# Optimization experiments

Measured on AMD Instinct MI355X. Metric: run time of the kernel, lower is better.

## Reference

```python
import jax, jax.numpy as jnp
import numpy as np

G = 200          # voxel grid extent per axis (spatial_shape)
EPS = 1e-5       # BatchNorm eps


def setup_inputs() -> dict:
    N, C_in, C_out = 1_000_000, 6, 32
    rng = np.random.default_rng(0)
    # unique active voxel sites (submanifold conv assumes deduplicated coords)
    lin = rng.choice(G ** 3, size=N, replace=False)
    coords = np.stack([lin // (G * G), (lin // G) % G, lin % G], axis=1).astype(np.int32)
    key = jax.random.key(0)
    k1, k2 = jax.random.split(key)
    feat = jax.random.normal(k1, (N, C_in), jnp.float32)
    W = jax.random.normal(k2, (27, C_in, C_out), jnp.float32) * (1.0 / np.sqrt(27 * C_in))
    gamma = jnp.ones((C_out,), jnp.float32)
    beta = jnp.zeros((C_out,), jnp.float32)
    return {"feat": feat, "coords": jnp.asarray(coords), "W": W, "gamma": gamma, "beta": beta}


def _subm_conv_bn_relu(feat, coords, W, gamma, beta):
    # Submanifold 3x3x3 sparse conv: output only at active sites.
    N = feat.shape[0]
    c = coords
    keys = (c[:, 0] * G + c[:, 1]) * G + c[:, 2]          # linearized voxel keys
    order = jnp.argsort(keys)
    skeys = keys[order]
    sfeat = feat[order]
    # all 27 kernel offsets, center included
    r = jnp.arange(-1, 2, dtype=c.dtype)
    offs = jnp.stack(jnp.meshgrid(r, r, r, indexing="ij"), -1).reshape(27, 3)

    def step(acc, xs):
        off, Wk = xs                                       # off: [3], Wk: [C_in, C_out]
        nc = c + off                                       # neighbor coords [N,3]
        valid = jnp.all((nc >= 0) & (nc < G), axis=1)
        nkey = (nc[:, 0] * G + nc[:, 1]) * G + nc[:, 2]
        pos = jnp.clip(jnp.searchsorted(skeys, nkey), 0, N - 1)
        found = valid & (skeys[pos] == nkey)               # rulebook hit mask
        g = jnp.where(found[:, None], sfeat[pos], 0.0)     # gathered neighbor feats [N,C_in]
        return acc + g @ Wk, None

    out, _ = jax.lax.scan(step, jnp.zeros((N, W.shape[2]), feat.dtype), (offs, W))
    # BatchNorm1d (training-mode batch stats) + ReLU
    mean = out.mean(0)
    var = out.var(0)
    out = (out - mean) * jax.lax.rsqrt(var + EPS) * gamma + beta
    return jax.nn.relu(out)


def reference(feat, coords, W, gamma, beta):
    return _subm_conv_bn_relu(feat, coords, W, gamma, beta)
```

## Files before the change

### kernel.cpp

```cpp
#include <hip/hip_runtime.h>
#include <stdint.h>

#define GRIDX 200
#define P 202
#define PCELL (P * P * P)
#define GUARD 100000
#define NBITS (PCELL + GUARD)
#define NWP ((NBITS + 31) / 32)
#define K_INV (PCELL + 50000)
#define CIN 6
#define COUT 32
#define NOFF 27
#define BN_EPS 1e-5f
#define WPB 1024
#define NBLKP ((NWP + WPB - 1) / WPB)

typedef __attribute__((ext_vector_type(8))) short short8;
typedef __attribute__((ext_vector_type(4))) float f32x4;


__device__ __forceinline__ int xcd_swizzle(int b, int nwg) {
    int q = nwg >> 3, r = nwg & 7;
    int xcd = b & 7, idx = b >> 3;
    int base = (xcd < r) ? xcd * (q + 1) : r * (q + 1) + (xcd - r) * q;
    return base + idx;
}

__device__ __forceinline__ unsigned short f2bf(float f) {
    uint32_t u = __float_as_uint(f);
    return (unsigned short)((u + 0x7FFFu + ((u >> 16) & 1u)) >> 16);
}
__device__ __forceinline__ uint32_t pack2(float a, float b) {
    return (uint32_t)f2bf(a) | ((uint32_t)f2bf(b) << 16);
}

__device__ __forceinline__ int koff_delta(int koff) {
    int t9 = koff / 9;
    int r9 = koff - t9 * 9;
    int t3 = r9 / 3;
    return (t9 - 1) * (P * P) + (t3 - 1) * P + (r9 - t3 * 3 - 1);
}


__global__ void build_bitmap_p(const int* __restrict__ coords, int N,
                               uint2* __restrict__ recs) {
    int i = blockIdx.x * blockDim.x + threadIdx.x;
    if (i >= N) return;
    int x = coords[3 * i], y = coords[3 * i + 1], z = coords[3 * i + 2];
    int key = ((x + 1) * P + (y + 1)) * P + (z + 1);
    atomicOr((unsigned int*)&recs[key >> 5], 1u << (key & 31));
}

__global__ __launch_bounds__(256)
void bitmap_count_p(const uint2* __restrict__ recs, int* __restrict__ bcnt) {
    __shared__ int tot[256];
    int b = blockIdx.x, t = threadIdx.x;
    int w0 = b * WPB + t * 4;
    int s = 0;
#pragma unroll
    for (int j = 0; j < 4; j++) {
        int w = w0 + j;
        if (w < NWP) s += __popc(recs[w].x);
    }
    tot[t] = s;
    __syncthreads();
    if (t < 128) tot[t] += tot[t + 128];
    __syncthreads();
    if (t < 64) {
        int v = tot[t] + tot[t + 64];
#pragma unroll
        for (int d = 32; d > 0; d >>= 1) v += __shfl_down(v, d);
        if (t == 0) bcnt[b] = v;
    }
}

__global__ void scan_small(const int* __restrict__ cnt, int* __restrict__ base, int n) {
    __shared__ int tot[256];
    int t = threadIdx.x;
    int v = (t < n) ? cnt[t] : 0;
    tot[t] = v;
    __syncthreads();
    for (int d = 1; d < 256; d <<= 1) {
        int u = (t >= d) ? tot[t - d] : 0;
        __syncthreads();
        tot[t] += u;
        __syncthreads();
    }
    if (t < n) base[t] = tot[t] - v;
}

__global__ __launch_bounds__(256)
void base_fill_p(uint2* __restrict__ recs, const int* __restrict__ bbase) {
    __shared__ int tot[256];
    int b = blockIdx.x, t = threadIdx.x;
    int w0 = b * WPB + t * 4;
    int p[4];
    int s = 0;
#pragma unroll
    for (int j = 0; j < 4; j++) {
        int w = w0 + j;
        p[j] = (w < NWP) ? __popc(recs[w].x) : 0;
        s += p[j];
    }
    tot[t] = s;
    __syncthreads();
    for (int d = 1; d < 256; d <<= 1) {
        int u = (t >= d) ? tot[t - d] : 0;
        __syncthreads();
        tot[t] += u;
        __syncthreads();
    }
    int run = bbase[b] + tot[t] - s;
#pragma unroll
    for (int j = 0; j < 4; j++) {
        int w = w0 + j;
        if (w < NWP) recs[w].y = (uint32_t)run;
        run += p[j];
    }
}


__global__ __launch_bounds__(256)
void gen_skeys(const uint2* __restrict__ recs, int* __restrict__ skeys) {
    int w = blockIdx.x * blockDim.x + threadIdx.x;
    if (w >= NWP) return;
    uint2 rb = recs[w];
    uint32_t m = rb.x;
    int base = (int)rb.y;
    int key0 = w * 32;
    while (m) {
        int bit = __ffs((int)m) - 1;
        skeys[base++] = key0 + bit;
        m &= m - 1u;
    }
}


__global__ __launch_bounds__(256)
void rank_scatter_p(const int* __restrict__ coords, const float* __restrict__ feat, int N,
                    const uint2* __restrict__ recs,
                    int* __restrict__ sorig,
                    uint4* __restrict__ feat_bf) {
    int i = blockIdx.x * blockDim.x + threadIdx.x;
    if (i >= N) return;
    int x = coords[3 * i], y = coords[3 * i + 1], z = coords[3 * i + 2];
    int key = ((x + 1) * P + (y + 1)) * P + (z + 1);
    uint2 rb = recs[key >> 5];
    int bit = key & 31;
    int r = (int)(rb.y + (uint32_t)__popc(rb.x & ((1u << bit) - 1u)));
    sorig[r] = i;
    const float* fr = feat + (size_t)i * CIN;
    float2 a = *(const float2*)fr;
    float2 bb = *(const float2*)(fr + 2);
    float2 cc = *(const float2*)(fr + 4);
    uint4 u;
    u.x = pack2(a.x, a.y);
    u.y = pack2(bb.x, bb.y);
    u.z = pack2(cc.x, cc.y);
    u.w = 0u;
    feat_bf[r] = u;
}


__global__ void prep_wfrag(const float* __restrict__ W, uint4* __restrict__ wfrag) {
    int idx = blockIdx.x * blockDim.x + threadIdx.x;
    if (idx >= 7 * 2 * 64) return;
    int l = idx & 63;
    int nt = (idx >> 6) & 1;
    int ks = idx >> 7;
    int koff = (l >> 4) * 7 + ks;
    int col = nt * 16 + (l & 15);
    unsigned short v[8];
#pragma unroll
    for (int ci = 0; ci < 8; ci++) {
        float f = 0.f;
        if (ci < CIN && koff < NOFF) f = W[(koff * CIN + ci) * COUT + col];
        v[ci] = f2bf(f);
    }
    uint4 u;
    u.x = (uint32_t)v[0] | ((uint32_t)v[1] << 16);
    u.y = (uint32_t)v[2] | ((uint32_t)v[3] << 16);
    u.z = (uint32_t)v[4] | ((uint32_t)v[5] << 16);
    u.w = (uint32_t)v[6] | ((uint32_t)v[7] << 16);
    wfrag[idx] = u;
}


__global__ __launch_bounds__(256, 4)
void conv_mfma(const uint4* __restrict__ feat_bf,
               const int* __restrict__ skeys,
               const int* __restrict__ sorig,
               const uint4* __restrict__ wfrag,
               const uint2* __restrict__ recs, int N, int nsb,
               float* __restrict__ out,
               float* __restrict__ stats_g) {
    __shared__ __align__(16) float Clds[64 * 36];
    __shared__ float bstat[64];

    int tid = threadIdx.x;
    int w = tid >> 6, l = tid & 63;
    int col = l & 15;
    int rg = l >> 4;
    int kb = rg;

    if (tid < 64) bstat[tid] = 0.f;

    const short8* wf8 = (const short8*)wfrag;
    short8 bf0[7], bf1[7];
#pragma unroll
    for (int ks = 0; ks < 7; ks++) {
        bf0[ks] = wf8[(ks * 2 + 0) * 64 + l];
        bf1[ks] = wf8[(ks * 2 + 1) * 64 + l];
    }

    int b1 = (0x3123 >> (kb * 4)) & 0xF;
    int b2 = b1 + 3;
    int len0 = b1, len2 = 4 - b1;
    int koffC0 = kb * 7;
    int koffC1 = koffC0 + b1;
    int koffC2 = koffC0 + b2;
    int d0 = koff_delta(koffC0);
    int d1 = koff_delta(koffC1);
    bool padC2 = (koffC2 >= NOFF);
    int d2 = padC2 ? 0 : koff_delta(koffC2);

    const uint4* fb16 = (const uint4*)feat_bf;

    float as0 = 0.f, aq0 = 0.f, as1 = 0.f, aq1 = 0.f;

    for (int sb = blockIdx.x; sb < nsb; sb += gridDim.x) {
        int b = xcd_swizzle(sb, nsb);
        int bs = b * 64;
        int site = bs + w * 16 + col;
        int key = (site < N) ? skeys[site] : K_INV;

        int nkA = key + d0;
        int nkB = key + d1;
        int nkC = padC2 ? K_INV : key + d2;
        int waA = nkA >> 5, waB = nkB >> 5, waC = nkC >> 5;
        uint2 rA0 = recs[waA];
        uint2 rB0 = recs[waB];
        uint2 rC0 = recs[waC];
        uint2 rA1 = rA0, rB1 = rB0, rC1 = rC0;
        if (((nkA & 31) + len0) > 32) rA1 = recs[waA + 1];
        if (((nkB & 31) + 3) > 32)    rB1 = recs[waB + 1];
        if (((nkC & 31) + len2) > 32) rC1 = recs[waC + 1];

        short8 av[7];
#pragma unroll
        for (int ks = 0; ks < 7; ks++) {
            int c = (ks >= b1) + (ks >= b2);
            int nk = (c == 0) ? (nkA + ks)
                   : (c == 1) ? (nkB + (ks - b1))
                              : (nkC + (ks - b2));
            int wa  = (c == 0) ? waA : (c == 1) ? waB : waC;
            uint2 r0 = (c == 0) ? rA0 : (c == 1) ? rB0 : rC0;
            uint2 r1 = (c == 0) ? rA1 : (c == 1) ? rB1 : rC1;
            bool second = (nk >> 5) != wa;
            uint32_t wd = second ? r1.x : r0.x;
            uint32_t bw = second ? r1.y : r0.y;
            int p = nk & 31;
            bool hit = (wd >> p) & 1u;
            uint4 a4 = make_uint4(0u, 0u, 0u, 0u);
            if (hit) {
                int pos = (int)(bw + (uint32_t)__popc(wd & ((1u << p) - 1u)));
                a4 = fb16[pos];
            }
            av[ks] = *(const short8*)&a4;
        }

        f32x4 acc0 = {0.f, 0.f, 0.f, 0.f};
        f32x4 acc1 = {0.f, 0.f, 0.f, 0.f};
#pragma unroll
        for (int ks = 0; ks < 7; ks++) {
            acc0 = __builtin_amdgcn_mfma_f32_16x16x32_bf16(av[ks], bf0[ks], acc0, 0, 0, 0);
            acc1 = __builtin_amdgcn_mfma_f32_16x16x32_bf16(av[ks], bf1[ks], acc1, 0, 0, 0);
        }

        as0 += acc0[0] + acc0[1] + acc0[2] + acc0[3];
        aq0 += acc0[0]*acc0[0] + acc0[1]*acc0[1] + acc0[2]*acc0[2] + acc0[3]*acc0[3];
        as1 += acc1[0] + acc1[1] + acc1[2] + acc1[3];
        aq1 += acc1[0]*acc1[0] + acc1[1]*acc1[1] + acc1[2]*acc1[2] + acc1[3]*acc1[3];

        __syncthreads();
#pragma unroll
        for (int r = 0; r < 4; r++) {
            int s = w * 16 + rg * 4 + r;
            Clds[s * 36 + col] = acc0[r];
            Clds[s * 36 + col + 16] = acc1[r];
        }
        __syncthreads();

        int st = tid >> 2;
        int q = (tid & 3) * 2;
        int sr = bs + st;
        if (sr < N) {
            float4* gp = (float4*)(out + (size_t)sorig[sr] * COUT + q * 4);
            gp[0] = *(const float4*)&Clds[st * 36 + q * 4];
            gp[1] = *(const float4*)&Clds[st * 36 + q * 4 + 4];
        }
    }

    as0 += __shfl_xor(as0, 16); as0 += __shfl_xor(as0, 32);
    aq0 += __shfl_xor(aq0, 16); aq0 += __shfl_xor(aq0, 32);
    as1 += __shfl_xor(as1, 16); as1 += __shfl_xor(as1, 32);
    aq1 += __shfl_xor(aq1, 16); aq1 += __shfl_xor(aq1, 32);
    __syncthreads();
    if (l < 16) {
        atomicAdd(&bstat[col], as0);
        atomicAdd(&bstat[16 + col], as1);
        atomicAdd(&bstat[32 + col], aq0);
        atomicAdd(&bstat[48 + col], aq1);
    }
    __syncthreads();
    if (tid < 64) {
        int slice = blockIdx.x & 63;
        atomicAdd(&stats_g[slice * 64 + tid], bstat[tid]);
    }
}


__global__ void finalize_sliced(const float* __restrict__ stats_g,
                                const float* __restrict__ gamma,
                                const float* __restrict__ beta,
                                float invN, float* __restrict__ scsh) {
    int c = threadIdx.x;
    if (c < COUT) {
        float s = 0.f, q = 0.f;
        for (int sl = 0; sl < 64; sl++) {
            s += stats_g[sl * 64 + c];
            q += stats_g[sl * 64 + 32 + c];
        }
        float mean = s * invN;
        float var = q * invN - mean * mean;
        float sc = gamma[c] * rsqrtf(var + BN_EPS);
        scsh[c] = sc;
        scsh[COUT + c] = beta[c] - mean * sc;
    }
}

__global__ __launch_bounds__(256)
void norm_kernel(float* __restrict__ out, long total_vec,
                 const float* __restrict__ scaleshift) {
    __shared__ float sc[COUT], sh[COUT];
    for (int t = threadIdx.x; t < COUT; t += blockDim.x) {
        sc[t] = scaleshift[t];
        sh[t] = scaleshift[COUT + t];
    }
    __syncthreads();
    long stride = (long)gridDim.x * blockDim.x;
    float4* p = (float4*)out;
    for (long v = (long)blockIdx.x * blockDim.x + threadIdx.x; v < total_vec; v += stride) {
        int cbase = (int)(v & 7) * 4;
        float4 u = p[v];
        u.x = fmaxf(u.x * sc[cbase + 0] + sh[cbase + 0], 0.f);
        u.y = fmaxf(u.y * sc[cbase + 1] + sh[cbase + 1], 0.f);
        u.z = fmaxf(u.z * sc[cbase + 2] + sh[cbase + 2], 0.f);
        u.w = fmaxf(u.w * sc[cbase + 3] + sh[cbase + 3], 0.f);
        p[v] = u;
    }
}


extern "C" void kernel_launch(void* const* d_in, const int* in_sizes, int n_in,
                              void* d_out, int out_size, void* d_ws, size_t ws_size,
                              hipStream_t stream) {
    const float* feat   = (const float*)d_in[0];
    const int*   coords = (const int*)d_in[1];
    const float* W      = (const float*)d_in[2];
    const float* gamma  = (const float*)d_in[3];
    const float* beta   = (const float*)d_in[4];
    float* out = (float*)d_out;

    int N = in_sizes[0] / CIN;
    const int threads = 256;
    int blocksN = (N + threads - 1) / threads;
    int nsb = (N + 63) / 64;
    int cblocks = 1024;
    long total_vec = (long)N * COUT / 4;

    size_t a256 = 255;
    size_t recs_b     = (size_t)NWP * 8;
    size_t off_skeys  = (recs_b + a256) & ~a256;
    size_t off_featbf = (off_skeys + (size_t)N * 4 + a256) & ~a256;
    size_t off_sorig  = (off_featbf + (size_t)(N + 1) * 16 + a256) & ~a256;
    size_t off_bcnt   = (off_sorig + (size_t)N * 4 + a256) & ~a256;
    size_t off_bbase  = (off_bcnt + 256 * 4 + a256) & ~a256;
    size_t off_wfrag  = (off_bbase + 256 * 4 + a256) & ~a256;
    size_t off_stats  = (off_wfrag + (size_t)(7 * 2 * 64) * 16 + a256) & ~a256;
    size_t off_scsh   = off_stats + (size_t)64 * 64 * 4;

    uint2* recs  = (uint2*)d_ws;
    int*   skeys = (int*)((char*)d_ws + off_skeys);
    uint4* featb = (uint4*)((char*)d_ws + off_featbf);
    int*   sorig = (int*)((char*)d_ws + off_sorig);
    int*   bcnt  = (int*)((char*)d_ws + off_bcnt);
    int*   bbase = (int*)((char*)d_ws + off_bbase);
    uint4* wfrag = (uint4*)((char*)d_ws + off_wfrag);
    float* stats = (float*)((char*)d_ws + off_stats);
    float* scsh  = (float*)((char*)d_ws + off_scsh);

    hipMemsetAsync(recs, 0, recs_b, stream);
    hipMemsetAsync(stats, 0, (size_t)64 * 64 * 4, stream);
    prep_wfrag<<<4, threads, 0, stream>>>(W, wfrag);
    build_bitmap_p<<<blocksN, threads, 0, stream>>>(coords, N, recs);
    bitmap_count_p<<<NBLKP, threads, 0, stream>>>(recs, bcnt);
    scan_small<<<1, threads, 0, stream>>>(bcnt, bbase, NBLKP);
    base_fill_p<<<NBLKP, threads, 0, stream>>>(recs, bbase);
    gen_skeys<<<(NWP + threads - 1) / threads, threads, 0, stream>>>(recs, skeys);
    rank_scatter_p<<<blocksN, threads, 0, stream>>>(coords, feat, N, recs, sorig, featb);
    conv_mfma<<<cblocks, threads, 0, stream>>>(featb, skeys, sorig, wfrag, recs, N, nsb, out, stats);
    finalize_sliced<<<1, 64, 0, stream>>>(stats, gamma, beta, 1.0f / (float)N, scsh);
    norm_kernel<<<2048, threads, 0, stream>>>(out, total_vec, scsh);
}
```

Baseline: 195.9 us.

## Fuse skey generation into base fill, vectorize coord/feat loads, merge memsets

Moves sorted-key emission into the prefix-sum base_fill kernel, which removes the separate gen_skeys launch and its reread of the bitmap. The bitmap build and rank-scatter kernels now have each thread handle 4 points using int4/float4 vector loads. The workspace is reordered so the bitmap and BN stats are contiguous, which lets a single memset zero both. The cost is more per-thread serial work in base_fill (each thread walks up to 4 words) and fewer threads in the scatter kernels.

```diff
diff --git a/kernel.cpp b/kernel.cpp
--- a/kernel.cpp
+++ b/kernel.cpp
@@ -42,13 +42,29 @@
 }
 
 
-__global__ void build_bitmap_p(const int* __restrict__ coords, int N,
-                               uint2* __restrict__ recs) {
-    int i = blockIdx.x * blockDim.x + threadIdx.x;
-    if (i >= N) return;
-    int x = coords[3 * i], y = coords[3 * i + 1], z = coords[3 * i + 2];
-    int key = ((x + 1) * P + (y + 1)) * P + (z + 1);
-    atomicOr((unsigned int*)&recs[key >> 5], 1u << (key & 31));
+__global__ __launch_bounds__(256)
+void build_bitmap_v4(const int* __restrict__ coords, int N, uint2* __restrict__ recs) {
+    int t = blockIdx.x * blockDim.x + threadIdx.x;
+    int i0 = t * 4;
+    if (i0 >= N) return;
+    if (i0 + 4 <= N) {
+        const int4* c4 = (const int4*)(coords + (size_t)i0 * 3);
+        int4 ca = c4[0], cb = c4[1], cc = c4[2];
+        int cx[4] = {ca.x, ca.w, cb.z, cc.y};
+        int cy[4] = {ca.y, cb.x, cb.w, cc.z};
+        int cz[4] = {ca.z, cb.y, cc.x, cc.w};
+#pragma unroll
+        for (int s = 0; s < 4; s++) {
+            int key = ((cx[s] + 1) * P + (cy[s] + 1)) * P + (cz[s] + 1);
+            atomicOr((unsigned int*)&recs[key >> 5], 1u << (key & 31));
+        }
+    } else {
+        for (int i = i0; i < N; i++) {
+            int x = coords[3 * i], y = coords[3 * i + 1], z = coords[3 * i + 2];
+            int key = ((x + 1) * P + (y + 1)) * P + (z + 1);
+            atomicOr((unsigned int*)&recs[key >> 5], 1u << (key & 31));
+        }
+    }
 }
 
 __global__ __launch_bounds__(256)
@@ -90,16 +106,19 @@
 }
 
 __global__ __launch_bounds__(256)
-void base_fill_p(uint2* __restrict__ recs, const int* __restrict__ bbase) {
+void base_fill_skeys(uint2* __restrict__ recs, const int* __restrict__ bbase,
+                     int* __restrict__ skeys) {
     __shared__ int tot[256];
     int b = blockIdx.x, t = threadIdx.x;
     int w0 = b * WPB + t * 4;
+    uint32_t wd[4];
     int p[4];
     int s = 0;
 #pragma unroll
     for (int j = 0; j < 4; j++) {
         int w = w0 + j;
-        p[j] = (w < NWP) ? __popc(recs[w].x) : 0;
+        wd[j] = (w < NWP) ? recs[w].x : 0u;
+        p[j] = __popc(wd[j]);
         s += p[j];
     }
     tot[t] = s;
@@ -114,51 +133,73 @@
 #pragma unroll
     for (int j = 0; j < 4; j++) {
         int w = w0 + j;
-        if (w < NWP) recs[w].y = (uint32_t)run;
-        run += p[j];
+        if (w < NWP) {
+            recs[w].y = (uint32_t)run;
+            uint32_t m = wd[j];
+            int rr = run;
+            int k0 = w * 32;
+            while (m) {
+                int bit = __ffs((int)m) - 1;
+                skeys[rr++] = k0 + bit;
+                m &= m - 1u;
+            }
+            run += p[j];
+        }
     }
 }
 
 
 __global__ __launch_bounds__(256)
-void gen_skeys(const uint2* __restrict__ recs, int* __restrict__ skeys) {
-    int w = blockIdx.x * blockDim.x + threadIdx.x;
-    if (w >= NWP) return;
-    uint2 rb = recs[w];
-    uint32_t m = rb.x;
-    int base = (int)rb.y;
-    int key0 = w * 32;
-    while (m) {
-        int bit = __ffs((int)m) - 1;
-        skeys[base++] = key0 + bit;
-        m &= m - 1u;
-    }
-}
-
-
-__global__ __launch_bounds__(256)
-void rank_scatter_p(const int* __restrict__ coords, const float* __restrict__ feat, int N,
-                    const uint2* __restrict__ recs,
-                    int* __restrict__ sorig,
-                    uint4* __restrict__ feat_bf) {
-    int i = blockIdx.x * blockDim.x + threadIdx.x;
-    if (i >= N) return;
-    int x = coords[3 * i], y = coords[3 * i + 1], z = coords[3 * i + 2];
-    int key = ((x + 1) * P + (y + 1)) * P + (z + 1);
-    uint2 rb = recs[key >> 5];
-    int bit = key & 31;
-    int r = (int)(rb.y + (uint32_t)__popc(rb.x & ((1u << bit) - 1u)));
-    sorig[r] = i;
-    const float* fr = feat + (size_t)i * CIN;
-    float2 a = *(const float2*)fr;
-    float2 bb = *(const float2*)(fr + 2);
-    float2 cc = *(const float2*)(fr + 4);
-    uint4 u;
-    u.x = pack2(a.x, a.y);
-    u.y = pack2(bb.x, bb.y);
-    u.z = pack2(cc.x, cc.y);
-    u.w = 0u;
-    feat_bf[r] = u;
+void rank_scatter_v4(const int* __restrict__ coords, const float* __restrict__ feat, int N,
+                     const uint2* __restrict__ recs,
+                     int* __restrict__ sorig, uint4* __restrict__ feat_bf) {
+    int t = blockIdx.x * blockDim.x + threadIdx.x;
+    int i0 = t * 4;
+    if (i0 >= N) return;
+    if (i0 + 4 <= N) {
+        const int4* c4 = (const int4*)(coords + (size_t)i0 * 3);
+        int4 ca = c4[0], cb = c4[1], cc = c4[2];
+        int cx[4] = {ca.x, ca.w, cb.z, cc.y};
+        int cy[4] = {ca.y, cb.x, cb.w, cc.z};
+        int cz[4] = {ca.z, cb.y, cc.x, cc.w};
+        const float4* f4 = (const float4*)(feat + (size_t)i0 * 6);
+        float4 fa = f4[0], fb = f4[1], fc = f4[2], fd = f4[3], fe = f4[4], ff = f4[5];
+        float fs[4][6] = {
+            {fa.x, fa.y, fa.z, fa.w, fb.x, fb.y},
+            {fb.z, fb.w, fc.x, fc.y, fc.z, fc.w},
+            {fd.x, fd.y, fd.z, fd.w, fe.x, fe.y},
+            {fe.z, fe.w, ff.x, ff.y, ff.z, ff.w}};
+#pragma unroll
+        for (int s = 0; s < 4; s++) {
+            int key = ((cx[s] + 1) * P + (cy[s] + 1)) * P + (cz[s] + 1);
+            uint2 rb = recs[key >> 5];
+            int bit = key & 31;
+            int r = (int)(rb.y + (uint32_t)__popc(rb.x & ((1u << bit) - 1u)));
+            sorig[r] = i0 + s;
+            uint4 u;
+            u.x = pack2(fs[s][0], fs[s][1]);
+            u.y = pack2(fs[s][2], fs[s][3]);
+            u.z = pack2(fs[s][4], fs[s][5]);
+            u.w = 0u;
+            feat_bf[r] = u;
+        }
+    } else {
+        for (int i = i0; i < N; i++) {
+            int x = coords[3 * i], y = coords[3 * i + 1], z = coords[3 * i + 2];
+            int key = ((x + 1) * P + (y + 1)) * P + (z + 1);
+            uint2 rb = recs[key >> 5];
+            int bit = key & 31;
+            int r = (int)(rb.y + (uint32_t)__popc(rb.x & ((1u << bit) - 1u)));
+            sorig[r] = i;
+            const float* fr = feat + (size_t)i * CIN;
+            uint4 u;
+            u.x = pack2(fr[0], fr[1]);
+            u.y = pack2(fr[2], fr[3]);
+            u.z = pack2(fr[4], fr[5]);
+            u.w = 0u;
+            feat_bf[r] = u;
+        }
+    }
 }
 
 
@@ -374,41 +415,40 @@
 
     int N = in_sizes[0] / CIN;
     const int threads = 256;
-    int blocksN = (N + threads - 1) / threads;
+    int blocks4 = (N + 4 * threads - 1) / (4 * threads);
     int nsb = (N + 63) / 64;
     int cblocks = 1024;
     long total_vec = (long)N * COUT / 4;
 
     size_t a256 = 255;
     size_t recs_b     = (size_t)NWP * 8;
-    size_t off_skeys  = (recs_b + a256) & ~a256;
+    size_t off_stats  = (recs_b + a256) & ~a256;
+    size_t zero_bytes = off_stats + (size_t)64 * 64 * 4;
+    size_t off_scsh   = (zero_bytes + a256) & ~a256;
+    size_t off_skeys  = (off_scsh + 2 * COUT * 4 + a256) & ~a256;
     size_t off_featbf = (off_skeys + (size_t)N * 4 + a256) & ~a256;
     size_t off_sorig  = (off_featbf + (size_t)(N + 1) * 16 + a256) & ~a256;
     size_t off_bcnt   = (off_sorig + (size_t)N * 4 + a256) & ~a256;
     size_t off_bbase  = (off_bcnt + 256 * 4 + a256) & ~a256;
     size_t off_wfrag  = (off_bbase + 256 * 4 + a256) & ~a256;
-    size_t off_stats  = (off_wfrag + (size_t)(7 * 2 * 64) * 16 + a256) & ~a256;
-    size_t off_scsh   = off_stats + (size_t)64 * 64 * 4;
 
     uint2* recs  = (uint2*)d_ws;
+    float* stats = (float*)((char*)d_ws + off_stats);
+    float* scsh  = (float*)((char*)d_ws + off_scsh);
     int*   skeys = (int*)((char*)d_ws + off_skeys);
     uint4* featb = (uint4*)((char*)d_ws + off_featbf);
     int*   sorig = (int*)((char*)d_ws + off_sorig);
     int*   bcnt  = (int*)((char*)d_ws + off_bcnt);
     int*   bbase = (int*)((char*)d_ws + off_bbase);
     uint4* wfrag = (uint4*)((char*)d_ws + off_wfrag);
-    float* stats = (float*)((char*)d_ws + off_stats);
-    float* scsh  = (float*)((char*)d_ws + off_scsh);
-
-    hipMemsetAsync(recs, 0, recs_b, stream);
-    hipMemsetAsync(stats, 0, (size_t)64 * 64 * 4, stream);
+
+    hipMemsetAsync(d_ws, 0, zero_bytes, stream);
     prep_wfrag<<<4, threads, 0, stream>>>(W, wfrag);
-    build_bitmap_p<<<blocksN, threads, 0, stream>>>(coords, N, recs);
+    build_bitmap_v4<<<blocks4, threads, 0, stream>>>(coords, N, recs);
     bitmap_count_p<<<NBLKP, threads, 0, stream>>>(recs, bcnt);
     scan_small<<<1, threads, 0, stream>>>(bcnt, bbase, NBLKP);
-    base_fill_p<<<NBLKP, threads, 0, stream>>>(recs, bbase);
-    gen_skeys<<<(NWP + threads - 1) / threads, threads, 0, stream>>>(recs, skeys);
-    rank_scatter_p<<<blocksN, threads, 0, stream>>>(coords, feat, N, recs, sorig, featb);
+    base_fill_skeys<<<NBLKP, threads, 0, stream>>>(recs, bbase, skeys);
+    rank_scatter_v4<<<blocks4, threads, 0, stream>>>(coords, feat, N, recs, sorig, featb);
     conv_mfma<<<cblocks, threads, 0, stream>>>(featb, skeys, sorig, wfrag, recs, N, nsb, out, stats);
     finalize_sliced<<<1, 64, 0, stream>>>(stats, gamma, beta, 1.0f / (float)N, scsh);
     norm_kernel<<<2048, threads, 0, stream>>>(out, total_vec, scsh);
```

Measured after the change: 194.8 us. About the same (-0.6%).
